# Kernel tuning notes

Hardware: AMD Instinct MI355X
Metric: run time of the kernel (lower is better)

## Reference

```python
import jax, jax.numpy as jnp
import numpy as np

EPS = 1e-12  # F.normalize eps
G = 8        # groups (init g)
NC = 32      # num_cluster
LMD = 2


def _l2norm(v, axis):
    n = jnp.sqrt(jnp.sum(v * v, axis=axis, keepdims=True))
    return v / jnp.maximum(n, EPS)


def setup_inputs() -> dict:
    key = jax.random.key(0)
    ks = jax.random.split(key, 6)
    b, m, d = 32, 512, 1024
    d2 = LMD * d                 # 2048
    nd = d2 // G                 # 256 = new_dims
    x = jax.random.normal(ks[0], (b, m, d), dtype=jnp.float32)
    mask = jnp.ones((b, m), dtype=bool)
    # Linear params with torch-like fan-in scaling
    We = jax.random.normal(ks[1], (d2, d), dtype=jnp.float32) / np.sqrt(d)
    be = jnp.zeros((d2,), dtype=jnp.float32)
    W1 = jax.random.normal(ks[2], (G * NC, d2), dtype=jnp.float32) / np.sqrt(d2)
    b1 = jnp.zeros((G * NC,), dtype=jnp.float32)
    W2 = jax.random.normal(ks[3], (G, d2), dtype=jnp.float32) / np.sqrt(d2)
    b2 = jnp.zeros((G,), dtype=jnp.float32)
    centroid = jax.random.uniform(ks[4], (NC, nd), dtype=jnp.float32)
    return {"x": x, "mask": mask, "We": We, "be": be, "W1": W1, "b1": b1,
            "W2": W2, "b2": b2, "centroid": centroid}


def reference(x, mask, We, be, W1, b1, W2, b2, centroid):
    b, m, d = x.shape
    # BaseAggregator: L2 normalize along feature dim (mask unused)
    xn = _l2norm(x, axis=2)
    xe = jnp.einsum('bmd,ed->bme', xn, We) + be          # (b, m, lmd*d)
    a1 = jax.nn.softmax((jnp.einsum('bme,ke->bmk', xe, W1) + b1)
                        .reshape(b, m, G, NC), axis=3)   # (b, m, G, nc)
    a2 = jax.nn.softmax(jnp.einsum('bme,ge->bmg', xe, W2) + b2, axis=2)  # (b, m, G)
    xg = xe.reshape(b, m, G, -1)                         # (b, m, G, new_dims)
    # sum_nc a1*(x - c) = x*sum(a1) - a1@c = x - a1@c  (softmax sums to 1)
    cent = jnp.einsum('bmgk,kd->bmgd', a1, centroid)     # (b, m, G, new_dims)
    v = jnp.einsum('bmg,bmgd->bd', a2, xg - cent) / m    # sum over G, mean over m
    return _l2norm(v, axis=1)
```

## Files before the change

### kernel.cpp

```cpp
#include <hip/hip_runtime.h>
#include <hip/hip_bf16.h>
#include <stdint.h>

#define B_BATCH 32
#define M_SEQ   512
#define R_TOT   16384
#define D_IN    1024
#define E_DIM   2048
#define NCAT    384
#define NVALID  264
#define G_GRP   8
#define NC_CL   32
#define ND_     256

typedef float  f32x4 __attribute__((ext_vector_type(4)));
typedef short  s16x8 __attribute__((ext_vector_type(8)));

__device__ __forceinline__ uint16_t f2bf(float f) {
  uint32_t u = __builtin_bit_cast(uint32_t, f);
  uint32_t r = (u + 0x7fffu + ((u >> 16) & 1u)) >> 16;
  return (uint16_t)r;
}
__device__ __forceinline__ float bf2f(uint16_t u) {
  return __builtin_bit_cast(float, (uint32_t)u << 16);
}

__device__ __forceinline__ f32x4 mfma_bf16(s16x8 a, s16x8 b, f32x4 c) {
  asm("v_mfma_f32_16x16x32_bf16 %0, %1, %2, %0" : "+v"(c) : "v"(a), "v"(b));
  return c;
}

typedef __attribute__((address_space(3))) void lds_void_t;
typedef const __attribute__((address_space(1))) void gbl_void_t;
__device__ __forceinline__ void async_load16(const void* g, void* l) {
  __builtin_amdgcn_global_load_lds((gbl_void_t*)g, (lds_void_t*)l, 16, 0, 0);
}

__global__ void zero_buf(float* __restrict__ p, int n) {
  int i = blockIdx.x * blockDim.x + threadIdx.x;
  if (i < n) p[i] = 0.0f;
}

__global__ void cvt_bf16(const float* __restrict__ src, uint16_t* __restrict__ dst, int n) {
  int i = blockIdx.x * blockDim.x + threadIdx.x;
  if (i < n) dst[i] = f2bf(src[i]);
}

__global__ void build_wcat(const float* __restrict__ W1, const float* __restrict__ W2,
                           uint16_t* __restrict__ wcat) {
  int i = blockIdx.x * blockDim.x + threadIdx.x;
  if (i >= NCAT * E_DIM) return;
  int row = i >> 11, col = i & (E_DIM - 1);
  float v = 0.0f;
  if (row < 256) v = W1[i];
  else if (row < NVALID) v = W2[(row - 256) * E_DIM + col];
  wcat[i] = f2bf(v);
}

__global__ void build_bcat(const float* __restrict__ b1, const float* __restrict__ b2,
                           float* __restrict__ bcat) {
  int i = blockIdx.x * blockDim.x + threadIdx.x;
  if (i >= NCAT) return;
  float v = 0.0f;
  if (i < 256) v = b1[i];
  else if (i < NVALID) v = b2[i - 256];
  bcat[i] = v;
}

__global__ __launch_bounds__(256) void normalize_rows(const float* __restrict__ x,
                                                      uint16_t* __restrict__ xn) {
  const int r = blockIdx.x, tid = threadIdx.x;
  const float4* xr = (const float4*)(x + (size_t)r * D_IN);
  float4 v = xr[tid];
  float ss = v.x * v.x + v.y * v.y + v.z * v.z + v.w * v.w;
  #pragma unroll
  for (int m = 32; m; m >>= 1) ss += __shfl_xor(ss, m);
  __shared__ float wsum[4];
  if ((tid & 63) == 0) wsum[tid >> 6] = ss;
  __syncthreads();
  float tot = wsum[0] + wsum[1] + wsum[2] + wsum[3];
  float scale = 1.0f / fmaxf(sqrtf(tot), 1e-12f);
  uint16_t* o = xn + (size_t)r * D_IN + tid * 4;
  o[0] = f2bf(v.x * scale); o[1] = f2bf(v.y * scale);
  o[2] = f2bf(v.z * scale); o[3] = f2bf(v.w * scale);
}

template <typename OutT>
__global__ __launch_bounds__(256, 2) void gemm_bt(
    const uint16_t* __restrict__ A, const uint16_t* __restrict__ B,
    const float* __restrict__ bias, OutT* __restrict__ C, int N, int K) {
  __shared__ __align__(16) uint16_t As[128 * 64];
  __shared__ __align__(16) uint16_t Bs[128 * 64];
  const int tid = threadIdx.x;
  const int w = tid >> 6, lane = tid & 63;
  const int wr = w >> 1, wc = w & 1;
  const int tm = blockIdx.x, tn = blockIdx.y;

  f32x4 acc[4][4] = {};

  const int lrow = lane >> 3;
  const int lk = (lane & 7) * 8;
  const size_t a_row0 = (size_t)tm * 128;
  const size_t b_row0 = (size_t)tn * 128;

  for (int k0 = 0; k0 < K; k0 += 64) {
    #pragma unroll
    for (int j = 0; j < 4; ++j) {
      const int c = w * 4 + j;
      const int row = c * 8 + lrow;
      async_load16(A + (a_row0 + row) * K + k0 + lk, (void*)(As + c * 512));
      async_load16(B + (b_row0 + row) * K + k0 + lk, (void*)(Bs + c * 512));
    }
    __syncthreads();
    #pragma unroll
    for (int kk = 0; kk < 2; ++kk) {
      const int krow = kk * 32 + (lane >> 4) * 8;
      s16x8 af[4], bfr[4];
      #pragma unroll
      for (int mi = 0; mi < 4; ++mi)
        af[mi] = *(const s16x8*)&As[(wr * 64 + mi * 16 + (lane & 15)) * 64 + krow];
      #pragma unroll
      for (int ni = 0; ni < 4; ++ni)
        bfr[ni] = *(const s16x8*)&Bs[(wc * 64 + ni * 16 + (lane & 15)) * 64 + krow];
      #pragma unroll
      for (int mi = 0; mi < 4; ++mi)
        #pragma unroll
        for (int ni = 0; ni < 4; ++ni)
          acc[mi][ni] = mfma_bf16(af[mi], bfr[ni], acc[mi][ni]);
    }
    __syncthreads();
  }
  asm volatile("s_nop 7\n\ts_nop 7\n\ts_nop 7" ::);

  const int rbase = wr * 64 + (lane >> 4) * 4;
  const int cbase = wc * 64 + (lane & 15);
  #pragma unroll
  for (int ni = 0; ni < 4; ++ni) {
    const int col = tn * 128 + cbase + ni * 16;
    const float bv = bias[col];
    #pragma unroll
    for (int mi = 0; mi < 4; ++mi) {
      #pragma unroll
      for (int jj = 0; jj < 4; ++jj) {
        const int row = tm * 128 + rbase + mi * 16 + jj;
        float v = acc[mi][ni][jj] + bv;
        if constexpr (sizeof(OutT) == 2) C[(size_t)row * N + col] = (OutT)f2bf(v);
        else                             C[(size_t)row * N + col] = v;
      }
    }
  }
}

__global__ __launch_bounds__(256) void softmax_accum(
    const float* __restrict__ logits,
    const uint16_t* __restrict__ xe,
    float* __restrict__ t1,
    float* __restrict__ sacc) {
  const int tid = threadIdx.x;
  const int r0 = blockIdx.x * 32;
  const int b = r0 >> 9;
  __shared__ float p1s[256];
  __shared__ float a2s[8];
  float t1_local = 0.0f, s_local = 0.0f;

  for (int rr = 0; rr < 32; ++rr) {
    const int r = r0 + rr;
    const float* lrow = logits + (size_t)r * NCAT;
    float lg = lrow[tid];
    float mx = lg;
    #pragma unroll
    for (int m = 16; m; m >>= 1) mx = fmaxf(mx, __shfl_xor(mx, m));
    float e = __expf(lg - mx);
    float sm = e;
    #pragma unroll
    for (int m = 16; m; m >>= 1) sm += __shfl_xor(sm, m);
    p1s[tid] = e / sm;
    if (tid < 8) {
      float l2 = lrow[256 + tid];
      float m2 = l2;
      #pragma unroll
      for (int m = 4; m; m >>= 1) m2 = fmaxf(m2, __shfl_xor(m2, m));
      float e2 = __expf(l2 - m2);
      float s2 = e2;
      #pragma unroll
      for (int m = 4; m; m >>= 1) s2 += __shfl_xor(s2, m);
      a2s[tid] = e2 / s2;
    }
    __syncthreads();
    const uint16_t* xr = xe + (size_t)r * E_DIM;
    float a = 0.0f;
    #pragma unroll
    for (int g = 0; g < 8; ++g) a += a2s[g] * bf2f(xr[g * 256 + tid]);
    t1_local += a;
    if (tid < 32) {
      float sa = 0.0f;
      #pragma unroll
      for (int g = 0; g < 8; ++g) sa += a2s[g] * p1s[g * 32 + tid];
      s_local += sa;
    }
    __syncthreads();
  }
  atomicAdd(&t1[b * 256 + tid], t1_local);
  if (tid < 32) atomicAdd(&sacc[b * 32 + tid], s_local);
}

__global__ __launch_bounds__(256) void finalize(const float* __restrict__ t1,
                                                const float* __restrict__ sacc,
                                                const float* __restrict__ centroid,
                                                float* __restrict__ out) {
  const int b = blockIdx.x, tid = threadIdx.x;
  float cs = 0.0f;
  #pragma unroll
  for (int k = 0; k < 32; ++k) cs += sacc[b * 32 + k] * centroid[k * 256 + tid];
  float v = (t1[b * 256 + tid] - cs) * (1.0f / (float)M_SEQ);
  float ss = v * v;
  #pragma unroll
  for (int m = 32; m; m >>= 1) ss += __shfl_xor(ss, m);
  __shared__ float wsum[4];
  if ((tid & 63) == 0) wsum[tid >> 6] = ss;
  __syncthreads();
  float tot = wsum[0] + wsum[1] + wsum[2] + wsum[3];
  out[b * 256 + tid] = v / fmaxf(sqrtf(tot), 1e-12f);
}

extern "C" void kernel_launch(void* const* d_in, const int* in_sizes, int n_in,
                              void* d_out, int out_size, void* d_ws, size_t ws_size,
                              hipStream_t stream) {
  const float* x        = (const float*)d_in[0];
  const float* We       = (const float*)d_in[2];
  const float* be       = (const float*)d_in[3];
  const float* W1       = (const float*)d_in[4];
  const float* b1       = (const float*)d_in[5];
  const float* W2       = (const float*)d_in[6];
  const float* b2       = (const float*)d_in[7];
  const float* centroid = (const float*)d_in[8];
  float* out = (float*)d_out;

  char* ws = (char*)d_ws;
  uint16_t* xe     = (uint16_t*)(ws + 0);
  uint16_t* xn     = (uint16_t*)(ws + 67108864);
  float*    logits = (float*)  (ws + 67108864);
  uint16_t* webf   = (uint16_t*)(ws + 100663296);
  uint16_t* wcat   = (uint16_t*)(ws + 104857600);
  float*    bcat   = (float*)  (ws + 106430464);
  float*    t1     = (float*)  (ws + 106432000);
  float*    sacc   = (float*)  (ws + 106464768);

  zero_buf  <<<dim3(36),   256, 0, stream>>>(t1, 8192 + 1024);
  cvt_bf16  <<<dim3(8192), 256, 0, stream>>>(We, webf, E_DIM * D_IN);
  build_wcat<<<dim3(3072), 256, 0, stream>>>(W1, W2, wcat);
  build_bcat<<<dim3(2),    256, 0, stream>>>(b1, b2, bcat);

  normalize_rows<<<dim3(R_TOT), 256, 0, stream>>>(x, xn);
  gemm_bt<uint16_t><<<dim3(R_TOT / 128, E_DIM / 128), 256, 0, stream>>>(
      xn, webf, be, xe, E_DIM, D_IN);
  gemm_bt<float><<<dim3(R_TOT / 128, NCAT / 128), 256, 0, stream>>>(
      xe, wcat, bcat, logits, NCAT, E_DIM);
  softmax_accum<<<dim3(R_TOT / 32), 256, 0, stream>>>(logits, xe, t1, sacc);
  finalize<<<dim3(B_BATCH), 256, 0, stream>>>(t1, sacc, centroid, out);
}
```

Measured before the change: 306.6 us.

## Replace first GEMM with 256x256-tile 8-wave pipelined MFMA kernel

Adds a gemm256 kernel for the xn@We^T projection. It uses 256x256 output tiles, 512 threads, a double-buffered XOR-swizzled LDS layout and async global-to-LDS loads. The loads are interleaved with MFMA phases separated by barriers and s_setprio. Larger tiles are meant to raise data reuse per LDS byte and hide load latency behind compute, at the cost of 128KB of LDS per block, higher register pressure, and fragile hand-scheduled waitcnt logic.

```diff
diff --git a/kernel.cpp b/kernel.cpp
--- a/kernel.cpp
+++ b/kernel.cpp
@@ -9,9 +9,6 @@
 #define E_DIM   2048
 #define NCAT    384
 #define NVALID  264
-#define G_GRP   8
-#define NC_CL   32
-#define ND_     256
 
 typedef float  f32x4 __attribute__((ext_vector_type(4)));
 typedef short  s16x8 __attribute__((ext_vector_type(8)));
@@ -35,6 +32,19 @@
 __device__ __forceinline__ void async_load16(const void* g, void* l) {
   __builtin_amdgcn_global_load_lds((gbl_void_t*)g, (lds_void_t*)l, 16, 0, 0);
 }
+
+#define FENCE() __builtin_amdgcn_sched_barrier(0)
+#define PH_PRE() do { FENCE(); __builtin_amdgcn_s_barrier(); FENCE(); \
+                      asm volatile("s_waitcnt lgkmcnt(0)" ::: "memory"); FENCE(); \
+                      __builtin_amdgcn_s_setprio(1); } while (0)
+#define PH_POST() do { __builtin_amdgcn_s_setprio(0); FENCE(); \
+                       __builtin_amdgcn_s_barrier(); FENCE(); } while (0)
+#define PH_POST_VM4() do { __builtin_amdgcn_s_setprio(0); FENCE(); \
+                       asm volatile("s_waitcnt vmcnt(4)" ::: "memory"); FENCE(); \
+                       __builtin_amdgcn_s_barrier(); FENCE(); } while (0)
+#define PH_POST_VM0() do { __builtin_amdgcn_s_setprio(0); FENCE(); \
+                       asm volatile("s_waitcnt vmcnt(0)" ::: "memory"); FENCE(); \
+                       __builtin_amdgcn_s_barrier(); FENCE(); } while (0)
 
 __global__ void zero_buf(float* __restrict__ p, int n) {
   int i = blockIdx.x * blockDim.x + threadIdx.x;
@@ -83,6 +93,122 @@
   uint16_t* o = xn + (size_t)r * D_IN + tid * 4;
   o[0] = f2bf(v.x * scale); o[1] = f2bf(v.y * scale);
   o[2] = f2bf(v.z * scale); o[3] = f2bf(v.w * scale);
+}
+
+template <int KDIM>
+__global__ __launch_bounds__(512, 2) void gemm256(
+    const uint16_t* __restrict__ A, const uint16_t* __restrict__ B,
+    const float* __restrict__ bias, uint16_t* __restrict__ C, int N) {
+  __shared__ uint16_t lds[65536];
+  constexpr int NT = KDIM / 64;
+  const int tid = threadIdx.x;
+  const int w = tid >> 6, lane = tid & 63;
+  const int wr = w >> 2, wc = w & 3;
+  const int bm = blockIdx.x, bn = blockIdx.y;
+
+  const int srow = tid >> 3;
+  const int scol = (((tid & 7) ^ (srow & 7)) << 3);
+  const int l15 = lane & 15, l4 = lane >> 4, lx = lane & 7;
+  const int ck0 = ((l4) ^ lx) << 4;
+  const int ck1 = ((4 + l4) ^ lx) << 4;
+
+  const int arow0 = bm * 256, brow0 = bn * 256;
+
+  auto STAGE = [&](const uint16_t* __restrict__ M, int grow0, int tile,
+                   int bufi, int mat, int half) {
+    if (tile >= NT) return;
+    const uint16_t* src = M + (size_t)(grow0 + half * 128 + srow) * KDIM + tile * 64 + scol;
+    uint16_t* dst = lds + ((bufi * 2 + mat) * 2 + half) * 8192 + w * 512;
+    async_load16(src, dst);
+    async_load16(src + (size_t)64 * KDIM, dst + 4096);
+  };
+  auto LDA = [&](int bufi, int mi, int ckb) -> s16x8 {
+    return *(const s16x8*)((const char*)(lds + ((bufi * 2 + 0) * 2 + wr) * 8192)
+                           + (mi * 16 + l15) * 128 + ckb);
+  };
+  auto LDB = [&](int bufi, int ni, int ckb) -> s16x8 {
+    return *(const s16x8*)((const char*)(lds + ((bufi * 2 + 1) * 2 + (wc >> 1)) * 8192)
+                           + ((wc & 1) * 64 + ni * 16 + l15) * 128 + ckb);
+  };
+
+  f32x4 acc[8][4] = {};
+  s16x8 aF[4][2], bF[4][2];
+
+  STAGE(A, arow0, 0, 0, 0, 0); STAGE(A, arow0, 0, 0, 0, 1);
+  STAGE(B, brow0, 0, 0, 1, 0); STAGE(B, brow0, 0, 0, 1, 1);
+  STAGE(B, brow0, 1, 1, 1, 0); STAGE(B, brow0, 1, 1, 1, 1);
+  asm volatile("s_waitcnt vmcnt(4)" ::: "memory");
+  __builtin_amdgcn_s_barrier(); FENCE();
+
+  for (int i = 0; i < NT / 2; ++i) {
+    const bool last = (i == NT / 2 - 1);
+    #pragma unroll
+    for (int h = 0; h < 2; ++h) {
+      const int T = 2 * i + h;
+      #pragma unroll
+      for (int mi = 0; mi < 4; ++mi) { aF[mi][0] = LDA(h, mi, ck0); aF[mi][1] = LDA(h, mi, ck1); }
+      #pragma unroll
+      for (int ni = 0; ni < 2; ++ni) { bF[ni][0] = LDB(h, ni, ck0); bF[ni][1] = LDB(h, ni, ck1); }
+      STAGE(A, arow0, T + 1, h ^ 1, 0, 0);
+      PH_PRE();
+      #pragma unroll
+      for (int mi = 0; mi < 4; ++mi)
+        #pragma unroll
+        for (int ni = 0; ni < 2; ++ni)
+          #pragma unroll
+          for (int kk = 0; kk < 2; ++kk)
+            acc[mi][ni] = mfma_bf16(aF[mi][kk], bF[ni][kk], acc[mi][ni]);
+      PH_POST();
+      #pragma unroll
+      for (int ni = 2; ni < 4; ++ni) { bF[ni][0] = LDB(h, ni, ck0); bF[ni][1] = LDB(h, ni, ck1); }
+      STAGE(A, arow0, T + 1, h ^ 1, 0, 1);
+      PH_PRE();
+      #pragma unroll
+      for (int mi = 0; mi < 4; ++mi)
+        #pragma unroll
+        for (int ni = 2; ni < 4; ++ni)
+          #pragma unroll
+          for (int kk = 0; kk < 2; ++kk)
+            acc[mi][ni] = mfma_bf16(aF[mi][kk], bF[ni][kk], acc[mi][ni]);
+      PH_POST();
+      #pragma unroll
+      for (int mi = 0; mi < 4; ++mi) { aF[mi][0] = LDA(h, 4 + mi, ck0); aF[mi][1] = LDA(h, 4 + mi, ck1); }
+      STAGE(B, brow0, T + 2, h, 1, 0);
+      PH_PRE();
+      #pragma unroll
+      for (int mi = 0; mi < 4; ++mi)
+        #pragma unroll
+        for (int ni = 0; ni < 2; ++ni)
+          #pragma unroll
+          for (int kk = 0; kk < 2; ++kk)
+            acc[4 + mi][ni] = mfma_bf16(aF[mi][kk], bF[ni][kk], acc[4 + mi][ni]);
+      PH_POST();
+      STAGE(B, brow0, T + 2, h, 1, 1);
+      PH_PRE();
+      #pragma unroll
+      for (int mi = 0; mi < 4; ++mi)
+        #pragma unroll
+        for (int ni = 2; ni < 4; ++ni)
+          #pragma unroll
+          for (int kk = 0; kk < 2; ++kk)
+            acc[4 + mi][ni] = mfma_bf16(aF[mi][kk], bF[ni][kk], acc[4 + mi][ni]);
+      if (last) { PH_POST_VM0(); } else { PH_POST_VM4(); }
+    }
+  }
+
+  asm volatile("s_nop 7\n\ts_nop 7\n\ts_nop 7" ::);
+  const int rb = arow0 + wr * 128 + l4 * 4;
+  const int cb = bn * 256 + wc * 64 + l15;
+  #pragma unroll
+  for (int ni = 0; ni < 4; ++ni) {
+    const int col = cb + ni * 16;
+    const float bv = bias[col];
+    #pragma unroll
+    for (int mi = 0; mi < 8; ++mi)
+      #pragma unroll
+      for (int jj = 0; jj < 4; ++jj)
+        C[(size_t)(rb + mi * 16 + jj) * N + col] = f2bf(acc[mi][ni][jj] + bv);
+  }
 }
 
 template <typename OutT>
@@ -252,8 +378,8 @@
   build_bcat<<<dim3(2),    256, 0, stream>>>(b1, b2, bcat);
 
   normalize_rows<<<dim3(R_TOT), 256, 0, stream>>>(x, xn);
-  gemm_bt<uint16_t><<<dim3(R_TOT / 128, E_DIM / 128), 256, 0, stream>>>(
-      xn, webf, be, xe, E_DIM, D_IN);
+  gemm256<D_IN><<<dim3(R_TOT / 256, E_DIM / 256), 512, 0, stream>>>(
+      xn, webf, be, xe, E_DIM);
   gemm_bt<float><<<dim3(R_TOT / 128, NCAT / 128), 256, 0, stream>>>(
       xe, wcat, bcat, logits, NCAT, E_DIM);
   softmax_accum<<<dim3(R_TOT / 32), 256, 0, stream>>>(logits, xe, t1, sacc);
```

Result: no change. 300.9 us (-1.8%).
